# Optimization experiments

Hardware: AMD Instinct MI355X
Metric: run time of the kernel (lower is better)

Reference implementation:

```python
import jax, jax.numpy as jnp
import numpy as np

B, S, E, H = 4, 2048, 1024, 16
D = E // H  # head_dim = 64

def setup_inputs() -> dict:
    key = jax.random.key(0)
    k1, k2, k3 = jax.random.split(key, 3)
    x = jax.random.normal(k1, (B, S, E), dtype=jnp.float32)
    # Linear weights stored as [in, out] so y = x @ W (torch Linear uses W^T; same math).
    w_att = jax.random.normal(k2, (E, 3 * E), dtype=jnp.float32) * (1.0 / np.sqrt(E))
    w_proj = jax.random.normal(k3, (E, E), dtype=jnp.float32) * (1.0 / np.sqrt(E))
    return {"x": x, "w_att": w_att, "w_proj": w_proj}

def reference(x, w_att, w_proj):
    b, s, e = x.shape
    qkv = x @ w_att                      # [b, s, 3e]
    q, k, v = jnp.split(qkv, 3, axis=-1)
    # [b, h, s, d]
    q = q.reshape(b, s, H, D).transpose(0, 2, 1, 3)
    k = k.reshape(b, s, H, D).transpose(0, 2, 1, 3)
    v = v.reshape(b, s, H, D).transpose(0, 2, 1, 3)
    scale = 1.0 / np.sqrt(D)
    att = jnp.einsum('bhqd,bhkd->bhqk', q, k) * scale  # [b, h, s, s]
    causal = jnp.tril(jnp.ones((s, s), dtype=bool))
    att = jnp.where(causal[None, None], att, jnp.finfo(att.dtype).min)
    att = jax.nn.softmax(att, axis=-1)
    y = jnp.einsum('bhqk,bhkd->bhqd', att, v)          # [b, h, s, d]
    y = y.transpose(0, 2, 1, 3).reshape(b, s, e)
    return y @ w_proj
```

## Files before the change

kernel.cpp:

```cpp
#include <hip/hip_runtime.h>
#include <hip/hip_bf16.h>

typedef __bf16 b16v8 __attribute__((ext_vector_type(8)));
typedef __bf16 b16v4 __attribute__((ext_vector_type(4)));
typedef float  f32x4 __attribute__((ext_vector_type(4)));

#define BB 4
#define SS 2048
#define EE 1024
#define HH 16
#define DD 64

#define QSCALE 0.18033688011112042f
#define CMAX 20.0f

__device__ __forceinline__ void async16(const __bf16* g, __bf16* l) {
  typedef __attribute__((address_space(1))) const unsigned int gu32;
  typedef __attribute__((address_space(3))) unsigned int lu32;
  __builtin_amdgcn_global_load_lds((gu32*)g, (lu32*)l, 16, 0, 0);
}

__device__ __forceinline__ f32x4 mfma16x16x16_bf16(b16v4 a, b16v4 b, f32x4 c) {
#if __has_builtin(__builtin_amdgcn_mfma_f32_16x16x16_bf16)
  return __builtin_amdgcn_mfma_f32_16x16x16_bf16(a, b, c, 0, 0, 0);
#else
  typedef short s16v4 __attribute__((ext_vector_type(4)));
  union U { b16v4 h; s16v4 s; };
  U ua, ub; ua.h = a; ub.h = b;
  return __builtin_amdgcn_mfma_f32_16x16x16bf16_1k(ua.s, ub.s, c, 0, 0, 0);
#endif
}

__global__ __launch_bounds__(256) void cast_x_kernel(const float* __restrict__ in,
                                                     __bf16* __restrict__ out, int n4) {
  int i = blockIdx.x * 256 + threadIdx.x;
  if (i >= n4) return;
  float4 f = ((const float4*)in)[i];
  b16v4 o = {(__bf16)f.x, (__bf16)f.y, (__bf16)f.z, (__bf16)f.w};
  ((b16v4*)out)[i] = o;
}

__global__ __launch_bounds__(256) void cast_transpose(const float* __restrict__ w,
                                                      __bf16* __restrict__ wt, int K, int N) {
  __shared__ float t[32][33];
  int n0 = blockIdx.x * 32, k0 = blockIdx.y * 32;
  int tx = threadIdx.x & 31, ty = threadIdx.x >> 5;
#pragma unroll
  for (int j = 0; j < 32; j += 8)
    t[ty + j][tx] = w[(size_t)(k0 + ty + j) * N + n0 + tx];
  __syncthreads();
#pragma unroll
  for (int j = 0; j < 32; j += 8)
    wt[(size_t)(n0 + ty + j) * K + k0 + tx] = (__bf16)t[tx][ty + j];
}

template <int EPI>
__global__ __launch_bounds__(256) void gemm_bt(const __bf16* __restrict__ A,
                                               const __bf16* __restrict__ Bt,
                                               void* C0, void* C1, void* C2,
                                               int M, int N, int K) {
  __shared__ __bf16 a_lds[2][128 * 32];
  __shared__ __bf16 b_lds[2][128 * 32];
  const int tid = threadIdx.x;
  const int lane = tid & 63;
  const int w = tid >> 6;
  const int wm = (w >> 1) * 64, wn = (w & 1) * 64;
  const int l16 = lane & 15, quad = lane >> 4;

  const int gx = gridDim.x;
  const int nwg = gx * gridDim.y;
  const int bid0 = blockIdx.y * gx + blockIdx.x;
  const int qq = nwg >> 3, rr = nwg & 7;
  const int xcd = bid0 & 7, idx = bid0 >> 3;
  const int wgid = (xcd < rr ? xcd * (qq + 1) : rr * (qq + 1) + (xcd - rr) * qq) + idx;
  const int bxx = wgid % gx, byy = wgid / gx;

  const __bf16* Ab = A + (size_t)byy * 128 * K;
  const __bf16* Bb = Bt + (size_t)bxx * 128 * K;

  auto stage = [&](int k0, int bufi) {
#pragma unroll
    for (int i = 0; i < 2; ++i) {
      int c = tid + i * 256;
      int row = c >> 2, ch = c & 3;
      async16(Ab + (size_t)row * K + k0 + ((ch ^ (row & 3)) * 8), a_lds[bufi] + c * 8);
    }
#pragma unroll
    for (int i = 0; i < 2; ++i) {
      int c = tid + i * 256;
      int row = c >> 2, ch = c & 3;
      async16(Bb + (size_t)row * K + k0 + ((ch ^ (row & 3)) * 8), b_lds[bufi] + c * 8);
    }
  };

  f32x4 acc[4][4];
#pragma unroll
  for (int i = 0; i < 4; ++i)
#pragma unroll
    for (int j = 0; j < 4; ++j) acc[i][j] = f32x4{0.f, 0.f, 0.f, 0.f};

  stage(0, 0);
  const int KT = K >> 5;
  const int sw = (quad ^ (l16 & 3)) * 8;
  for (int kt = 0; kt < KT; ++kt) {
    __syncthreads();
    if (kt + 1 < KT) stage((kt + 1) << 5, (kt + 1) & 1);
    const __bf16* ab = a_lds[kt & 1];
    const __bf16* bb = b_lds[kt & 1];
    b16v8 af[4], bf4[4];
#pragma unroll
    for (int t = 0; t < 4; ++t) {
      af[t] = *(const b16v8*)(ab + (wm + t * 16 + l16) * 32 + sw);
      bf4[t] = *(const b16v8*)(bb + (wn + t * 16 + l16) * 32 + sw);
    }
#pragma unroll
    for (int mt = 0; mt < 4; ++mt)
#pragma unroll
      for (int nt = 0; nt < 4; ++nt)
        acc[mt][nt] = __builtin_amdgcn_mfma_f32_16x16x32_bf16(af[mt], bf4[nt], acc[mt][nt], 0, 0, 0);
  }

  if (EPI == 0) {
    __bf16* qb = (__bf16*)C0;
    __bf16* kb = (__bf16*)C1;
    __bf16* vtb = (__bf16*)C2;
#pragma unroll
    for (int mt = 0; mt < 4; ++mt)
#pragma unroll
      for (int nt = 0; nt < 4; ++nt) {
        int row = byy * 128 + wm + mt * 16 + quad * 4;
        int col = bxx * 128 + wn + nt * 16 + l16;
        int b = row >> 11, s = row & 2047;
        int sec = col >> 10, cc = col & 1023;
        int h = cc >> 6, d = cc & 63;
        if (sec == 2) {
          b16v4 vv = {(__bf16)acc[mt][nt][0], (__bf16)acc[mt][nt][1],
                      (__bf16)acc[mt][nt][2], (__bf16)acc[mt][nt][3]};
          *(b16v4*)(vtb + ((size_t)(b * HH + h) * DD + d) * SS + s) = vv;
        } else {
          __bf16* dst = (sec == 0) ? qb : kb;
          float sc = (sec == 0) ? QSCALE : 1.0f;
#pragma unroll
          for (int r = 0; r < 4; ++r)
            dst[(((size_t)(b * HH + h) * SS + s + r) << 6) + d] = (__bf16)(acc[mt][nt][r] * sc);
        }
      }
  } else {
    float* out = (float*)C0;
#pragma unroll
    for (int mt = 0; mt < 4; ++mt)
#pragma unroll
      for (int nt = 0; nt < 4; ++nt)
#pragma unroll
        for (int r = 0; r < 4; ++r) {
          int row = byy * 128 + wm + mt * 16 + quad * 4 + r;
          int col = bxx * 128 + wn + nt * 16 + l16;
          out[(size_t)row * N + col] = acc[mt][nt][r];
        }
  }
}

__global__ __launch_bounds__(256, 4) void attn_kernel(const __bf16* __restrict__ qb,
                                                      const __bf16* __restrict__ kb,
                                                      const __bf16* __restrict__ vtb,
                                                      __bf16* __restrict__ y) {
  __shared__ __bf16 kv_lds[2][8192];
  const int tid = threadIdx.x;
  const int lane = tid & 63;
  const int w = tid >> 6;
  const int l16 = lane & 15, quad = lane >> 4;
  const int bh = blockIdx.x, p = blockIdx.y;
  const int b = bh >> 4, h = bh & 15;
  const __bf16* kbase = kb + (size_t)bh * SS * DD;
  const __bf16* vtbase = vtb + (size_t)bh * DD * SS;

  const int e = l16 & 7;
  const int koff0 = l16 * 64 + ((quad ^ e) * 8);
  const int koff1 = l16 * 64 + (((quad + 4) ^ e) * 8);
  int voff[4];
#pragma unroll
  for (int kf = 0; kf < 4; ++kf)
    voff[kf] = 4096 + l16 * 64 + (((kf * 2 + (quad >> 1)) ^ e) * 8) + ((quad & 1) * 4);

  int gK[2], gV[2], lK[2], lV[2];
#pragma unroll
  for (int i = 0; i < 2; ++i) {
    int L = tid + i * 256;
    int row = L >> 3, c = L & 7;
    gK[i] = row * DD + ((c ^ (row & 7)) * 8);
    lK[i] = L * 8;
    gV[i] = row * SS + ((c ^ (row & 7)) * 8);
    lV[i] = 4096 + L * 8;
  }
  auto stage = [&](int j, __bf16* buf) {
    const __bf16* kj = kbase + j * (64 * DD);
    const __bf16* vj = vtbase + j * 64;
#pragma unroll
    for (int i = 0; i < 2; ++i) async16(kj + gK[i], buf + lK[i]);
#pragma unroll
    for (int i = 0; i < 2; ++i) async16(vj + gV[i], buf + lV[i]);
  };

#pragma unroll
  for (int t = 0; t < 2; ++t) {
    const int qt = (t == 0) ? (31 - p) : p;

    b16v8 qf[2];
#pragma unroll
    for (int ks = 0; ks < 2; ++ks)
      qf[ks] = *(const b16v8*)(qb + ((size_t)bh * SS + qt * 64 + w * 16 + l16) * DD + ks * 32 + quad * 8);

    f32x4 o[4];
#pragma unroll
    for (int dt = 0; dt < 4; ++dt) o[dt] = f32x4{0.f, 0.f, 0.f, 0.f};
    f32x4 lv = {0.f, 0.f, 0.f, 0.f};

    __syncthreads();
    stage(0, kv_lds[0]);

    for (int j = 0; j <= qt; ++j) {
      __syncthreads();
      if (j < qt) stage(j + 1, kv_lds[(j + 1) & 1]);
      const __bf16* buf = kv_lds[0] + ((j & 1) << 13);

      f32x4 s[4];
#pragma unroll
      for (int kf = 0; kf < 4; ++kf) s[kf] = f32x4{-CMAX, -CMAX, -CMAX, -CMAX};
      __builtin_amdgcn_s_setprio(1);
#pragma unroll
      for (int kf = 0; kf < 4; ++kf) {
        b16v8 k0 = *(const b16v8*)(buf + koff0 + kf * 1024);
        b16v8 k1 = *(const b16v8*)(buf + koff1 + kf * 1024);
        s[kf] = __builtin_amdgcn_mfma_f32_16x16x32_bf16(k0, qf[0], s[kf], 0, 0, 0);
        s[kf] = __builtin_amdgcn_mfma_f32_16x16x32_bf16(k1, qf[1], s[kf], 0, 0, 0);
      }
      __builtin_amdgcn_s_setprio(0);
      if (j == qt) {
        int ql = w * 16 + l16;
#pragma unroll
        for (int kf = 0; kf < 4; ++kf)
#pragma unroll
          for (int r = 0; r < 4; ++r)
            if (kf * 16 + quad * 4 + r > ql) s[kf][r] = -1e30f;
      }
#pragma unroll
      for (int kf = 0; kf < 4; ++kf)
#pragma unroll
        for (int r = 0; r < 4; ++r) s[kf][r] = __builtin_amdgcn_exp2f(s[kf][r]);
      lv += (s[0] + s[1]) + (s[2] + s[3]);
      __builtin_amdgcn_s_setprio(1);
#pragma unroll
      for (int kf = 0; kf < 4; ++kf) {
        b16v4 pf = {(__bf16)s[kf][0], (__bf16)s[kf][1], (__bf16)s[kf][2], (__bf16)s[kf][3]};
#pragma unroll
        for (int dt = 0; dt < 4; ++dt) {
          b16v4 vf = *(const b16v4*)(buf + voff[kf] + dt * 1024);
          o[dt] = mfma16x16x16_bf16(vf, pf, o[dt]);
        }
      }
      __builtin_amdgcn_s_setprio(0);
    }

    float lr = (lv[0] + lv[1]) + (lv[2] + lv[3]);
    lr += __shfl_xor(lr, 16);
    lr += __shfl_xor(lr, 32);
    float inv = 1.0f / lr;
    int q = qt * 64 + w * 16 + l16;
#pragma unroll
    for (int dt = 0; dt < 4; ++dt) {
      b16v4 ov = {(__bf16)(o[dt][0] * inv), (__bf16)(o[dt][1] * inv),
                  (__bf16)(o[dt][2] * inv), (__bf16)(o[dt][3] * inv)};
      *(b16v4*)(y + ((size_t)b * SS + q) * EE + h * 64 + dt * 16 + quad * 4) = ov;
    }
  }
}

extern "C" void kernel_launch(void* const* d_in, const int* in_sizes, int n_in,
                              void* d_out, int out_size, void* d_ws, size_t ws_size,
                              hipStream_t stream) {
  (void)in_sizes; (void)n_in; (void)out_size; (void)ws_size;
  const float* x = (const float*)d_in[0];
  const float* w_att = (const float*)d_in[1];
  const float* w_proj = (const float*)d_in[2];
  float* out = (float*)d_out;

  char* ws = (char*)d_ws;
  size_t off = 0;
  auto alloc = [&](size_t elems) { __bf16* p = (__bf16*)(ws + off); off += elems * 2; return p; };
  __bf16* xb = alloc(8388608);
  __bf16* qb = alloc(8388608);
  __bf16* kb = alloc(8388608);
  __bf16* vtb = alloc(8388608);
  __bf16* watt = alloc(3145728);
  __bf16* wproj = alloc(1048576);

  cast_x_kernel<<<8192, 256, 0, stream>>>(x, xb, 2097152);
  cast_transpose<<<dim3(96, 32), 256, 0, stream>>>(w_att, watt, 1024, 3072);
  cast_transpose<<<dim3(32, 32), 256, 0, stream>>>(w_proj, wproj, 1024, 1024);
  gemm_bt<0><<<dim3(24, 64), 256, 0, stream>>>(xb, watt, qb, kb, vtb, 8192, 3072, 1024);
  attn_kernel<<<dim3(64, 16), 256, 0, stream>>>(qb, kb, vtb, xb);
  gemm_bt<1><<<dim3(8, 64), 256, 0, stream>>>(xb, wproj, out, nullptr, nullptr, 8192, 1024, 1024);
}
```

Before: 244.8 us.

## Fuse input cast kernels into one launch and use narrower N tile for output projection

```diff
diff --git a/kernel.cpp b/kernel.cpp
--- a/kernel.cpp
+++ b/kernel.cpp
@@ -31,19 +31,28 @@
 #endif
 }
 
-__global__ __launch_bounds__(256) void cast_x_kernel(const float* __restrict__ in,
-                                                     __bf16* __restrict__ out, int n4) {
-  int i = blockIdx.x * 256 + threadIdx.x;
-  if (i >= n4) return;
-  float4 f = ((const float4*)in)[i];
-  b16v4 o = {(__bf16)f.x, (__bf16)f.y, (__bf16)f.z, (__bf16)f.w};
-  ((b16v4*)out)[i] = o;
-}
-
-__global__ __launch_bounds__(256) void cast_transpose(const float* __restrict__ w,
-                                                      __bf16* __restrict__ wt, int K, int N) {
+__global__ __launch_bounds__(256) void prep_kernel(const float* __restrict__ x,
+                                                   __bf16* __restrict__ xb,
+                                                   const float* __restrict__ w_att,
+                                                   __bf16* __restrict__ watt,
+                                                   const float* __restrict__ w_proj,
+                                                   __bf16* __restrict__ wproj) {
   __shared__ float t[32][33];
-  int n0 = blockIdx.x * 32, k0 = blockIdx.y * 32;
+  const int bid = blockIdx.x;
+  if (bid < 8192) {
+    int i = bid * 256 + threadIdx.x;
+    float4 f = ((const float4*)x)[i];
+    b16v4 o = {(__bf16)f.x, (__bf16)f.y, (__bf16)f.z, (__bf16)f.w};
+    ((b16v4*)xb)[i] = o;
+    return;
+  }
+  const float* w;
+  __bf16* wt;
+  int N, local;
+  if (bid < 11264) { w = w_att; wt = watt; N = 3072; local = bid - 8192; }
+  else             { w = w_proj; wt = wproj; N = 1024; local = bid - 11264; }
+  const int K = 1024;
+  int n0 = (local % (N >> 5)) * 32, k0 = (local / (N >> 5)) * 32;
   int tx = threadIdx.x & 31, ty = threadIdx.x >> 5;
 #pragma unroll
   for (int j = 0; j < 32; j += 8)
@@ -54,18 +63,20 @@
     wt[(size_t)(n0 + ty + j) * K + k0 + tx] = (__bf16)t[tx][ty + j];
 }
 
-template <int EPI>
+template <int EPI, int BN>
 __global__ __launch_bounds__(256) void gemm_bt(const __bf16* __restrict__ A,
                                                const __bf16* __restrict__ Bt,
                                                void* C0, void* C1, void* C2,
                                                int M, int N, int K) {
   __shared__ __bf16 a_lds[2][128 * 32];
-  __shared__ __bf16 b_lds[2][128 * 32];
+  __shared__ __bf16 b_lds[2][BN * 32];
   const int tid = threadIdx.x;
   const int lane = tid & 63;
   const int w = tid >> 6;
-  const int wm = (w >> 1) * 64, wn = (w & 1) * 64;
+  const int wm = (w >> 1) * 64, wn = (w & 1) * (BN / 2);
   const int l16 = lane & 15, quad = lane >> 4;
+  constexpr int NT = BN / 64 + 1;
+  constexpr int NF = (BN == 128) ? 4 : 2;
 
   const int gx = gridDim.x;
   const int nwg = gx * gridDim.y;
@@ -76,7 +87,7 @@
   const int bxx = wgid % gx, byy = wgid / gx;
 
   const __bf16* Ab = A + (size_t)byy * 128 * K;
-  const __bf16* Bb = Bt + (size_t)bxx * 128 * K;
+  const __bf16* Bb = Bt + (size_t)bxx * BN * K;
 
   auto stage = [&](int k0, int bufi) {
 #pragma unroll
@@ -86,18 +97,18 @@
       async16(Ab + (size_t)row * K + k0 + ((ch ^ (row & 3)) * 8), a_lds[bufi] + c * 8);
     }
 #pragma unroll
-    for (int i = 0; i < 2; ++i) {
+    for (int i = 0; i < BN / 64; ++i) {
       int c = tid + i * 256;
       int row = c >> 2, ch = c & 3;
       async16(Bb + (size_t)row * K + k0 + ((ch ^ (row & 3)) * 8), b_lds[bufi] + c * 8);
     }
   };
 
-  f32x4 acc[4][4];
+  f32x4 acc[4][NF];
 #pragma unroll
   for (int i = 0; i < 4; ++i)
 #pragma unroll
-    for (int j = 0; j < 4; ++j) acc[i][j] = f32x4{0.f, 0.f, 0.f, 0.f};
+    for (int j = 0; j < NF; ++j) acc[i][j] = f32x4{0.f, 0.f, 0.f, 0.f};
 
   stage(0, 0);
   const int KT = K >> 5;
@@ -107,16 +118,17 @@
     if (kt + 1 < KT) stage((kt + 1) << 5, (kt + 1) & 1);
     const __bf16* ab = a_lds[kt & 1];
     const __bf16* bb = b_lds[kt & 1];
-    b16v8 af[4], bf4[4];
-#pragma unroll
-    for (int t = 0; t < 4; ++t) {
+    b16v8 af[4], bf4[NF];
+#pragma unroll
+    for (int t = 0; t < 4; ++t)
       af[t] = *(const b16v8*)(ab + (wm + t * 16 + l16) * 32 + sw);
+#pragma unroll
+    for (int t = 0; t < NF; ++t)
       bf4[t] = *(const b16v8*)(bb + (wn + t * 16 + l16) * 32 + sw);
-    }
 #pragma unroll
     for (int mt = 0; mt < 4; ++mt)
 #pragma unroll
-      for (int nt = 0; nt < 4; ++nt)
+      for (int nt = 0; nt < NF; ++nt)
         acc[mt][nt] = __builtin_amdgcn_mfma_f32_16x16x32_bf16(af[mt], bf4[nt], acc[mt][nt], 0, 0, 0);
   }
 
@@ -127,9 +139,9 @@
 #pragma unroll
     for (int mt = 0; mt < 4; ++mt)
 #pragma unroll
-      for (int nt = 0; nt < 4; ++nt) {
+      for (int nt = 0; nt < NF; ++nt) {
         int row = byy * 128 + wm + mt * 16 + quad * 4;
-        int col = bxx * 128 + wn + nt * 16 + l16;
+        int col = bxx * BN + wn + nt * 16 + l16;
         int b = row >> 11, s = row & 2047;
         int sec = col >> 10, cc = col & 1023;
         int h = cc >> 6, d = cc & 63;
@@ -150,11 +162,11 @@
 #pragma unroll
     for (int mt = 0; mt < 4; ++mt)
 #pragma unroll
-      for (int nt = 0; nt < 4; ++nt)
+      for (int nt = 0; nt < NF; ++nt)
 #pragma unroll
         for (int r = 0; r < 4; ++r) {
           int row = byy * 128 + wm + mt * 16 + quad * 4 + r;
-          int col = bxx * 128 + wn + nt * 16 + l16;
+          int col = bxx * BN + wn + nt * 16 + l16;
           out[(size_t)row * N + col] = acc[mt][nt][r];
         }
   }
@@ -294,10 +306,8 @@
   __bf16* watt = alloc(3145728);
   __bf16* wproj = alloc(1048576);
 
-  cast_x_kernel<<<8192, 256, 0, stream>>>(x, xb, 2097152);
-  cast_transpose<<<dim3(96, 32), 256, 0, stream>>>(w_att, watt, 1024, 3072);
-  cast_transpose<<<dim3(32, 32), 256, 0, stream>>>(w_proj, wproj, 1024, 1024);
-  gemm_bt<0><<<dim3(24, 64), 256, 0, stream>>>(xb, watt, qb, kb, vtb, 8192, 3072, 1024);
+  prep_kernel<<<12288, 256, 0, stream>>>(x, xb, w_att, watt, w_proj, wproj);
+  gemm_bt<0, 128><<<dim3(24, 64), 256, 0, stream>>>(xb, watt, qb, kb, vtb, 8192, 3072, 1024);
   attn_kernel<<<dim3(64, 16), 256, 0, stream>>>(qb, kb, vtb, xb);
-  gemm_bt<1><<<dim3(8, 64), 256, 0, stream>>>(xb, wproj, out, nullptr, nullptr, 8192, 1024, 1024);
-}
+  gemm_bt<1, 64><<<dim3(16, 64), 256, 0, stream>>>(xb, wproj, out, nullptr, nullptr, 8192, 1024, 1024);
+}
```

Result: faster. 239.3 us (-2.3%).
